# Kernel optimization log

Hardware: AMD Instinct MI355X
Metric: run time of the kernel (lower is better)

Reference implementation:

```python
import jax, jax.numpy as jnp
import numpy as np
from jax import lax

KH, KW = 3, 3
K = KH * KW
STRIDE, PAD, DIL = 1, 1, 1
CIN, COUT = 64, 64


def setup_inputs() -> dict:
    key = jax.random.key(0)
    k1, k2, k3, k4 = jax.random.split(key, 4)
    B, H, W = 8, 96, 96
    x = jax.random.normal(k1, (B, CIN, H, W), dtype=jnp.float32)
    # offset/mask conv params (small so sampled offsets stay near the grid)
    w_off = jax.random.normal(k2, (3 * K, CIN, KH, KW), dtype=jnp.float32) * 0.01
    b_off = jnp.zeros((3 * K,), dtype=jnp.float32)
    # main deformable conv weight, uniform(-stdv, stdv) like reset_parameters
    stdv = 1.0 / np.sqrt(CIN * KH * KW)
    weight = jax.random.uniform(k3, (COUT, CIN, KH, KW), dtype=jnp.float32,
                                minval=-stdv, maxval=stdv)
    bias = jax.random.normal(k4, (COUT,), dtype=jnp.float32) * 0.01
    return {"x": x, "w_off": w_off, "b_off": b_off, "weight": weight, "bias": bias}


def _bilinear_sample(img, ys, xs):
    # img: [C,H,W]; ys, xs: [K,Ho,Wo] float sample coords. Zero outside borders.
    C, H, W = img.shape
    y0 = jnp.floor(ys)
    x0 = jnp.floor(xs)
    wy1 = ys - y0  # weight for y0+1
    wx1 = xs - x0
    wy0 = 1.0 - wy1
    wx0 = 1.0 - wx1

    def gather(yi, xi):
        yc = jnp.clip(yi, 0, H - 1).astype(jnp.int32)
        xc = jnp.clip(xi, 0, W - 1).astype(jnp.int32)
        valid = ((yi >= 0) & (yi <= H - 1) & (xi >= 0) & (xi <= W - 1))
        # [C,K,Ho,Wo]
        return img[:, yc, xc] * valid.astype(img.dtype)[None]

    return (gather(y0, x0) * (wy0 * wx0)[None]
            + gather(y0, x0 + 1) * (wy0 * wx1)[None]
            + gather(y0 + 1, x0) * (wy1 * wx0)[None]
            + gather(y0 + 1, x0 + 1) * (wy1 * wx1)[None])


def reference(x, w_off, b_off, weight, bias):
    B, C, H, W = x.shape
    # offset/mask conv (same geometry as main conv)
    om = lax.conv_general_dilated(
        x, w_off, window_strides=(STRIDE, STRIDE),
        padding=[(PAD, PAD), (PAD, PAD)], rhs_dilation=(DIL, DIL),
        dimension_numbers=("NCHW", "OIHW", "NCHW")) + b_off[None, :, None, None]
    Ho, Wo = om.shape[2], om.shape[3]
    offset = om[:, :2 * K].reshape(B, K, 2, Ho, Wo)  # interleaved (dy,dx) per tap
    dy, dx = offset[:, :, 0], offset[:, :, 1]         # [B,K,Ho,Wo]
    mask = jax.nn.sigmoid(om[:, 2 * K:])              # [B,K,Ho,Wo]

    k = jnp.arange(K)
    ky = (k // KW).astype(jnp.float32) * DIL  # [K]
    kx = (k % KW).astype(jnp.float32) * DIL
    oy = jnp.arange(Ho, dtype=jnp.float32) * STRIDE - PAD  # [Ho]
    ox = jnp.arange(Wo, dtype=jnp.float32) * STRIDE - PAD  # [Wo]
    ys = oy[None, None, :, None] + ky[None, :, None, None] + dy  # [B,K,Ho,Wo]
    xs = ox[None, None, None, :] + kx[None, :, None, None] + dx

    sampled = jax.vmap(_bilinear_sample)(x, ys, xs)  # [B,C,K,Ho,Wo]
    w_r = weight.reshape(weight.shape[0], C, K)      # [O,C,K]
    out = jnp.einsum("bkhw,bckhw,ock->bohw", mask, sampled, w_r)
    return out + bias[None, :, None, None]
```

## Files before the change

kernel.cpp:

```cpp
#include <hip/hip_runtime.h>
#include <math.h>

typedef __bf16 b16x8 __attribute__((ext_vector_type(8)));
typedef float  f32x4 __attribute__((ext_vector_type(4)));

#define B_    8
#define CIN_  64
#define COUT_ 64
#define Hs    96
#define Ws    96
#define PLANE (Hs*Ws)
#define IMG   (CIN_*PLANE)
#define NP    (B_*PLANE)
#define NBLK  (NP/64)

#define WR 10
#define WC 24
#define WPIX (WR*WC)
#define WBYTES (WPIX*128)

__device__ __forceinline__ int swz(int bid) { return (bid & 7) * (NBLK / 8) + (bid >> 3); }

__global__ void prep_xpose(const float* __restrict__ x,
                           const float* __restrict__ weight, const float* __restrict__ w_off,
                           __bf16* __restrict__ xT,
                           __bf16* __restrict__ wAB, __bf16* __restrict__ wAO) {
    int bid = blockIdx.x;
    if (bid < 288) {
        int p = bid * 256 + threadIdx.x;
        int b = p / PLANE, r = p - b * PLANE;
        const float* src = x + b * IMG + r;
        __bf16 buf[64];
#pragma unroll
        for (int c = 0; c < 64; ++c) buf[c] = (__bf16)src[c * PLANE];
        b16x8* dst = (b16x8*)(xT + (size_t)p * 64);
#pragma unroll
        for (int j = 0; j < 8; ++j) dst[j] = ((const b16x8*)buf)[j];
    } else {
        int i = (bid - 288) * 256 + threadIdx.x;
        if (i < 36864) {
            int e = i & 7, lane = (i >> 3) & 63, mt = (i >> 9) & 3, ks = (i >> 11) & 1, k = i >> 12;
            int o = mt * 16 + (lane & 15);
            int c = ks * 32 + ((lane >> 4) << 3) + e;
            wAB[i] = (__bf16)weight[o * 576 + c * 9 + k];
        }
        if (i < 18432) {
            int e = i & 7, lane = (i >> 3) & 63, mt = (i >> 9) & 1, ks = (i >> 10) & 1, t = i >> 11;
            int ch = mt * 16 + (lane & 15);
            int c  = ks * 32 + ((lane >> 4) << 3) + e;
            wAO[i] = (ch < 27) ? (__bf16)w_off[ch * 576 + c * 9 + t] : (__bf16)(0.f);
        }
    }
}

__global__ __launch_bounds__(256, 4)
void deform_mfma(const __bf16* __restrict__ xT,
                 const __bf16* __restrict__ wAO,
                 const float* __restrict__ b_off,
                 const __bf16* __restrict__ wAB,
                 const float* __restrict__ bias,
                 float* __restrict__ out) {
    __shared__ __align__(16) unsigned char smemWin[WBYTES];
    __shared__ float omL[4][27 * 16];

    int tid  = threadIdx.x;
    int lane = tid & 63;
    int s    = __builtin_amdgcn_readfirstlane(tid >> 6);
    int n    = lane & 15;
    int q    = lane >> 4;

    int t    = swz(blockIdx.x);
    int b    = t / 144;
    int rem  = t - b * 144;
    int rq   = rem / 6;
    int ct   = rem - rq * 6;
    int h0   = rq * 4;
    int c0   = ct * 16;
    int hrow = h0 + s;
    int w    = c0 + n;

    const __bf16* xTimg = xT + (size_t)b * PLANE * 64;
    const __bf16* xTb   = xTimg + q * 8;

    const b16x8* wAOv = (const b16x8*)wAO;
    const b16x8* wABv = (const b16x8*)wAB;
    int boff = q * 16;

#define LDSRD(sl, off) (*(const b16x8*)(smemWin + (sl) * 128 + ((off) ^ (((sl) & 7) << 4))))

#pragma unroll
    for (int r2 = 0; r2 < 8; ++r2) {
        int idx = tid + r2 * 256;
        if (r2 < 7 || tid < (WPIX * 8 - 1792)) {
            int pix = idx >> 3, j = idx & 7;
            int yw = pix / WC, xw = pix - yw * WC;
            int ys = min(max(h0 - 3 + yw, 0), Hs - 1);
            int xs = min(max(c0 - 3 + xw, 0), Ws - 1);
            b16x8 v = *(const b16x8*)(xTimg + ((ys * Ws + xs) * 64) + j * 8);
            *(b16x8*)(smemWin + pix * 128 + ((j * 16) ^ ((pix & 7) << 4))) = v;
        }
    }
    __syncthreads();

    f32x4 accA0 = {0.f, 0.f, 0.f, 0.f};
    f32x4 accA1 = {0.f, 0.f, 0.f, 0.f};
    const b16x8 ZER = {};

#pragma unroll 3
    for (int tt = 0; tt < 9; ++tt) {
        int ky = tt / 3, kx = tt - ky * 3;
        int yy = hrow - 1 + ky, xx = w - 1 + kx;
        bool mk = (yy >= 0 && yy < Hs && xx >= 0 && xx < Ws);
        int sl = (s + 2 + ky) * WC + (n + 2 + kx);
        b16x8 bf0 = LDSRD(sl, boff);
        b16x8 bf1 = LDSRD(sl, boff + 64);
        bf0 = mk ? bf0 : ZER;
        bf1 = mk ? bf1 : ZER;
        b16x8 af0 = wAOv[((tt * 2 + 0) * 2 + 0) * 64 + lane];
        b16x8 af1 = wAOv[((tt * 2 + 0) * 2 + 1) * 64 + lane];
        b16x8 af2 = wAOv[((tt * 2 + 1) * 2 + 0) * 64 + lane];
        b16x8 af3 = wAOv[((tt * 2 + 1) * 2 + 1) * 64 + lane];
        accA0 = __builtin_amdgcn_mfma_f32_16x16x32_bf16(af0, bf0, accA0, 0, 0, 0);
        accA1 = __builtin_amdgcn_mfma_f32_16x16x32_bf16(af1, bf0, accA1, 0, 0, 0);
        accA0 = __builtin_amdgcn_mfma_f32_16x16x32_bf16(af2, bf1, accA0, 0, 0, 0);
        accA1 = __builtin_amdgcn_mfma_f32_16x16x32_bf16(af3, bf1, accA1, 0, 0, 0);
    }
    float* omW = &omL[s][0];
#pragma unroll
    for (int rg = 0; rg < 4; ++rg) { int ch = q * 4 + rg;      omW[ch * 16 + n] = accA0[rg] + b_off[ch]; }
#pragma unroll
    for (int rg = 0; rg < 4; ++rg) { int ch = 16 + q * 4 + rg; if (ch < 27) omW[ch * 16 + n] = accA1[rg] + b_off[ch]; }

    f32x4 acc0 = {0.f, 0.f, 0.f, 0.f};
    f32x4 acc1 = {0.f, 0.f, 0.f, 0.f};
    f32x4 acc2 = {0.f, 0.f, 0.f, 0.f};
    f32x4 acc3 = {0.f, 0.f, 0.f, 0.f};

#pragma unroll 3
    for (int k = 0; k < 9; ++k) {
        float dy = omW[(2 * k) * 16 + n];
        float dx = omW[(2 * k + 1) * 16 + n];
        float mo = omW[(18 + k) * 16 + n];

        float m  = 1.f / (1.f + __expf(-mo));
        int ky = k / 3, kx = k - ky * 3;
        float ysf = (float)(hrow - 1 + ky) + dy;
        float xsf = (float)(w    - 1 + kx) + dx;
        float y0f = floorf(ysf), x0f = floorf(xsf);
        float ly = ysf - y0f, lx = xsf - x0f;
        float hy = 1.f - ly, hx = 1.f - lx;
        int y0 = (int)y0f, x0 = (int)x0f, y1 = y0 + 1, x1 = x0 + 1;
        bool vy0 = (y0 >= 0) && (y0 < Hs), vy1 = (y1 >= 0) && (y1 < Hs);
        bool vx0 = (x0 >= 0) && (x0 < Ws), vx1 = (x1 >= 0) && (x1 < Ws);
        float W00 = (vy0 && vx0) ? m * hy * hx : 0.f;
        float W01 = (vy0 && vx1) ? m * hy * lx : 0.f;
        float W10 = (vy1 && vx0) ? m * ly * hx : 0.f;
        float W11 = (vy1 && vx1) ? m * ly * lx : 0.f;

        bool inw = (y0 >= h0 - 3) && (y1 <= h0 + 6) && (x0 >= c0 - 3) && (x1 <= c0 + 20);

        b16x8 e00, e01, e10, e11, o00, o01, o10, o11;
        if (inw) {
            int sl = (y0 - (h0 - 3)) * WC + (x0 - (c0 - 3));
            e00 = LDSRD(sl, boff);           o00 = LDSRD(sl, boff + 64);
            e01 = LDSRD(sl + 1, boff);       o01 = LDSRD(sl + 1, boff + 64);
            e10 = LDSRD(sl + WC, boff);      o10 = LDSRD(sl + WC, boff + 64);
            e11 = LDSRD(sl + WC + 1, boff);  o11 = LDSRD(sl + WC + 1, boff + 64);
        } else {
            int y0c = min(max(y0, 0), Hs - 1), y1c = min(max(y1, 0), Hs - 1);
            int x0c = min(max(x0, 0), Ws - 1), x1c = min(max(x1, 0), Ws - 1);
            const b16x8* P00 = (const b16x8*)(xTb + (y0c * Ws + x0c) * 64);
            const b16x8* P01 = (const b16x8*)(xTb + (y0c * Ws + x1c) * 64);
            const b16x8* P10 = (const b16x8*)(xTb + (y1c * Ws + x0c) * 64);
            const b16x8* P11 = (const b16x8*)(xTb + (y1c * Ws + x1c) * 64);
            e00 = P00[0]; o00 = P00[4];
            e01 = P01[0]; o01 = P01[4];
            e10 = P10[0]; o10 = P10[4];
            e11 = P11[0]; o11 = P11[4];
        }

        b16x8 a0 = wABv[(k * 8 + 0) * 64 + lane];
        b16x8 a1 = wABv[(k * 8 + 1) * 64 + lane];
        b16x8 a2 = wABv[(k * 8 + 2) * 64 + lane];
        b16x8 a3 = wABv[(k * 8 + 3) * 64 + lane];

        b16x8 fe;
#pragma unroll
        for (int j = 0; j < 8; ++j)
            fe[j] = (__bf16)((float)e00[j] * W00 + (float)e01[j] * W01 +
                             (float)e10[j] * W10 + (float)e11[j] * W11);
        acc0 = __builtin_amdgcn_mfma_f32_16x16x32_bf16(a0, fe, acc0, 0, 0, 0);
        acc1 = __builtin_amdgcn_mfma_f32_16x16x32_bf16(a1, fe, acc1, 0, 0, 0);
        acc2 = __builtin_amdgcn_mfma_f32_16x16x32_bf16(a2, fe, acc2, 0, 0, 0);
        acc3 = __builtin_amdgcn_mfma_f32_16x16x32_bf16(a3, fe, acc3, 0, 0, 0);

        b16x8 a4 = wABv[(k * 8 + 4) * 64 + lane];
        b16x8 a5 = wABv[(k * 8 + 5) * 64 + lane];
        b16x8 a6 = wABv[(k * 8 + 6) * 64 + lane];
        b16x8 a7 = wABv[(k * 8 + 7) * 64 + lane];

        b16x8 fo;
#pragma unroll
        for (int j = 0; j < 8; ++j)
            fo[j] = (__bf16)((float)o00[j] * W00 + (float)o01[j] * W01 +
                             (float)o10[j] * W10 + (float)o11[j] * W11);
        acc0 = __builtin_amdgcn_mfma_f32_16x16x32_bf16(a4, fo, acc0, 0, 0, 0);
        acc1 = __builtin_amdgcn_mfma_f32_16x16x32_bf16(a5, fo, acc1, 0, 0, 0);
        acc2 = __builtin_amdgcn_mfma_f32_16x16x32_bf16(a6, fo, acc2, 0, 0, 0);
        acc3 = __builtin_amdgcn_mfma_f32_16x16x32_bf16(a7, fo, acc3, 0, 0, 0);
    }
#undef LDSRD

    int ob = b * (COUT_ * PLANE) + hrow * Ws + w;
    f32x4 bs0 = *(const f32x4*)&bias[q * 4];
    f32x4 bs1 = *(const f32x4*)&bias[16 + q * 4];
    f32x4 bs2 = *(const f32x4*)&bias[32 + q * 4];
    f32x4 bs3 = *(const f32x4*)&bias[48 + q * 4];
#pragma unroll
    for (int rg = 0; rg < 4; ++rg) { int o =      q * 4 + rg; out[ob + o * PLANE] = acc0[rg] + bs0[rg]; }
#pragma unroll
    for (int rg = 0; rg < 4; ++rg) { int o = 16 + q * 4 + rg; out[ob + o * PLANE] = acc1[rg] + bs1[rg]; }
#pragma unroll
    for (int rg = 0; rg < 4; ++rg) { int o = 32 + q * 4 + rg; out[ob + o * PLANE] = acc2[rg] + bs2[rg]; }
#pragma unroll
    for (int rg = 0; rg < 4; ++rg) { int o = 48 + q * 4 + rg; out[ob + o * PLANE] = acc3[rg] + bs3[rg]; }
}

extern "C" void kernel_launch(void* const* d_in, const int* in_sizes, int n_in,
                              void* d_out, int out_size, void* d_ws, size_t ws_size,
                              hipStream_t stream) {
    const float* x      = (const float*)d_in[0];
    const float* w_off  = (const float*)d_in[1];
    const float* b_off  = (const float*)d_in[2];
    const float* weight = (const float*)d_in[3];
    const float* bias   = (const float*)d_in[4];
    float* out = (float*)d_out;

    char* ws = (char*)d_ws;
    __bf16* wAB = (__bf16*)ws;
    __bf16* wAO = (__bf16*)(ws + 73728);
    __bf16* xT  = (__bf16*)(ws + 131072);

    prep_xpose<<<432, 256, 0, stream>>>(x, weight, w_off, xT, wAB, wAO);
    deform_mfma<<<NBLK, 256, 0, stream>>>(xT, wAO, b_off, wAB, bias, out);
}
```

Before: 117.9 us.

## Shrink LDS halo window and software-pipeline bilinear tap loads across iterations

Shrinks the LDS input window from a 3-pixel to a 2-pixel halo (10x24 to 9x21 pixels, staged in exactly 6 passes with no tail guard), which cuts LDS footprint and staging loads. The deformable loop is restructured so the offset/weight math and even-half corner loads for tap k+1 are issued while tap k's odd half is being blended and fed to MFMA. The loop is no longer unrolled. Samples falling outside the smaller window take the global-memory fallback more often, and carrying the next tap's data raises register pressure.

```diff
diff --git a/kernel.cpp b/kernel.cpp
--- a/kernel.cpp
+++ b/kernel.cpp
@@ -14,10 +14,11 @@
 #define NP    (B_*PLANE)
 #define NBLK  (NP/64)
 
-#define WR 10
-#define WC 24
+#define WR 9
+#define WC 21
 #define WPIX (WR*WC)
-#define WBYTES (WPIX*128)
+#define WSTG 192
+#define WBYTES (WSTG*128)
 
 __device__ __forceinline__ int swz(int bid) { return (bid & 7) * (NBLK / 8) + (bid >> 3); }
 
@@ -86,19 +87,17 @@
     const b16x8* wABv = (const b16x8*)wAB;
     int boff = q * 16;
 
-#define LDSRD(sl, off) (*(const b16x8*)(smemWin + (sl) * 128 + ((off) ^ (((sl) & 7) << 4))))
-
-#pragma unroll
-    for (int r2 = 0; r2 < 8; ++r2) {
+#define LDSRD(sl_, off_) (*(const b16x8*)(smemWin + (sl_) * 128 + ((off_) ^ (((sl_) & 7) << 4))))
+
+#pragma unroll
+    for (int r2 = 0; r2 < 6; ++r2) {
         int idx = tid + r2 * 256;
-        if (r2 < 7 || tid < (WPIX * 8 - 1792)) {
-            int pix = idx >> 3, j = idx & 7;
-            int yw = pix / WC, xw = pix - yw * WC;
-            int ys = min(max(h0 - 3 + yw, 0), Hs - 1);
-            int xs = min(max(c0 - 3 + xw, 0), Ws - 1);
-            b16x8 v = *(const b16x8*)(xTimg + ((ys * Ws + xs) * 64) + j * 8);
-            *(b16x8*)(smemWin + pix * 128 + ((j * 16) ^ ((pix & 7) << 4))) = v;
-        }
+        int pix = idx >> 3, j = idx & 7;
+        int yw = pix / WC, xw = pix - yw * WC;
+        int ys = min(max(h0 - 2 + yw, 0), Hs - 1);
+        int xs = min(max(c0 - 2 + xw, 0), Ws - 1);
+        b16x8 v = *(const b16x8*)(xTimg + ((ys * Ws + xs) * 64) + j * 8);
+        *(b16x8*)(smemWin + pix * 128 + ((j * 16) ^ ((pix & 7) << 4))) = v;
     }
     __syncthreads();
 
@@ -111,9 +110,9 @@
         int ky = tt / 3, kx = tt - ky * 3;
         int yy = hrow - 1 + ky, xx = w - 1 + kx;
         bool mk = (yy >= 0 && yy < Hs && xx >= 0 && xx < Ws);
-        int sl = (s + 2 + ky) * WC + (n + 2 + kx);
-        b16x8 bf0 = LDSRD(sl, boff);
-        b16x8 bf1 = LDSRD(sl, boff + 64);
+        int slA = (s + 1 + ky) * WC + (n + 1 + kx);
+        b16x8 bf0 = LDSRD(slA, boff);
+        b16x8 bf1 = LDSRD(slA, boff + 64);
         bf0 = mk ? bf0 : ZER;
         bf1 = mk ? bf1 : ZER;
         b16x8 af0 = wAOv[((tt * 2 + 0) * 2 + 0) * 64 + lane];
@@ -136,53 +135,67 @@
     f32x4 acc2 = {0.f, 0.f, 0.f, 0.f};
     f32x4 acc3 = {0.f, 0.f, 0.f, 0.f};
 
-#pragma unroll 3
+    float W00, W01, W10, W11;
+    int   sl, y0r, x0r;
+    bool  inw;
+    b16x8 e00, e01, e10, e11;
+
+#define CALC_FROM(dy, dx, mo, kk) do {                                            \
+        float m  = 1.f / (1.f + __expf(-(mo)));                                   \
+        int ky = (kk) / 3, kx = (kk) - ky * 3;                                    \
+        float ysf = (float)(hrow - 1 + ky) + (dy);                                \
+        float xsf = (float)(w    - 1 + kx) + (dx);                                \
+        float y0f = floorf(ysf), x0f = floorf(xsf);                               \
+        float ly = ysf - y0f, lx = xsf - x0f;                                     \
+        float hy = 1.f - ly, hx = 1.f - lx;                                       \
+        y0r = (int)y0f; x0r = (int)x0f;                                           \
+        int y1 = y0r + 1, x1 = x0r + 1;                                           \
+        bool vy0 = (y0r >= 0) && (y0r < Hs), vy1 = (y1 >= 0) && (y1 < Hs);        \
+        bool vx0 = (x0r >= 0) && (x0r < Ws), vx1 = (x1 >= 0) && (x1 < Ws);        \
+        W00 = (vy0 && vx0) ? m * hy * hx : 0.f;                                   \
+        W01 = (vy0 && vx1) ? m * hy * lx : 0.f;                                   \
+        W10 = (vy1 && vx0) ? m * ly * hx : 0.f;                                   \
+        W11 = (vy1 && vx1) ? m * ly * lx : 0.f;                                   \
+        inw = (y0r >= h0 - 2) && (y1 <= h0 + 6) && (x0r >= c0 - 2) && (x1 <= c0 + 18); \
+        sl  = (y0r - (h0 - 2)) * WC + (x0r - (c0 - 2));                           \
+    } while (0)
+
+#define LOAD4(d0, d1, d2, d3, OFF, ELO) do {                                      \
+        if (inw) {                                                                \
+            d0 = LDSRD(sl, OFF);          d1 = LDSRD(sl + 1, OFF);                \
+            d2 = LDSRD(sl + WC, OFF);     d3 = LDSRD(sl + WC + 1, OFF);           \
+        } else {                                                                  \
+            int y0c = min(max(y0r, 0), Hs - 1), y1c = min(max(y0r + 1, 0), Hs - 1); \
+            int x0c = min(max(x0r, 0), Ws - 1), x1c = min(max(x0r + 1, 0), Ws - 1); \
+            d0 = *(const b16x8*)(xTb + (y0c * Ws + x0c) * 64 + (ELO));            \
+            d1 = *(const b16x8*)(xTb + (y0c * Ws + x1c) * 64 + (ELO));            \
+            d2 = *(const b16x8*)(xTb + (y1c * Ws + x0c) * 64 + (ELO));            \
+            d3 = *(const b16x8*)(xTb + (y1c * Ws + x1c) * 64 + (ELO));            \
+        }                                                                         \
+    } while (0)
+
+    {
+        float dy0 = omW[0 * 16 + n], dx0 = omW[1 * 16 + n], mo0 = omW[18 * 16 + n];
+        CALC_FROM(dy0, dx0, mo0, 0);
+        LOAD4(e00, e01, e10, e11, boff, 0);
+    }
+
+#pragma unroll 1
     for (int k = 0; k < 9; ++k) {
-        float dy = omW[(2 * k) * 16 + n];
-        float dx = omW[(2 * k + 1) * 16 + n];
-        float mo = omW[(18 + k) * 16 + n];
-
-        float m  = 1.f / (1.f + __expf(-mo));
-        int ky = k / 3, kx = k - ky * 3;
-        float ysf = (float)(hrow - 1 + ky) + dy;
-        float xsf = (float)(w    - 1 + kx) + dx;
-        float y0f = floorf(ysf), x0f = floorf(xsf);
-        float ly = ysf - y0f, lx = xsf - x0f;
-        float hy = 1.f - ly, hx = 1.f - lx;
-        int y0 = (int)y0f, x0 = (int)x0f, y1 = y0 + 1, x1 = x0 + 1;
-        bool vy0 = (y0 >= 0) && (y0 < Hs), vy1 = (y1 >= 0) && (y1 < Hs);
-        bool vx0 = (x0 >= 0) && (x0 < Ws), vx1 = (x1 >= 0) && (x1 < Ws);
-        float W00 = (vy0 && vx0) ? m * hy * hx : 0.f;
-        float W01 = (vy0 && vx1) ? m * hy * lx : 0.f;
-        float W10 = (vy1 && vx0) ? m * ly * hx : 0.f;
-        float W11 = (vy1 && vx1) ? m * ly * lx : 0.f;
-
-        bool inw = (y0 >= h0 - 3) && (y1 <= h0 + 6) && (x0 >= c0 - 3) && (x1 <= c0 + 20);
-
-        b16x8 e00, e01, e10, e11, o00, o01, o10, o11;
-        if (inw) {
-            int sl = (y0 - (h0 - 3)) * WC + (x0 - (c0 - 3));
-            e00 = LDSRD(sl, boff);           o00 = LDSRD(sl, boff + 64);
-            e01 = LDSRD(sl + 1, boff);       o01 = LDSRD(sl + 1, boff + 64);
-            e10 = LDSRD(sl + WC, boff);      o10 = LDSRD(sl + WC, boff + 64);
-            e11 = LDSRD(sl + WC + 1, boff);  o11 = LDSRD(sl + WC + 1, boff + 64);
-        } else {
-            int y0c = min(max(y0, 0), Hs - 1), y1c = min(max(y1, 0), Hs - 1);
-            int x0c = min(max(x0, 0), Ws - 1), x1c = min(max(x1, 0), Ws - 1);
-            const b16x8* P00 = (const b16x8*)(xTb + (y0c * Ws + x0c) * 64);
-            const b16x8* P01 = (const b16x8*)(xTb + (y0c * Ws + x1c) * 64);
-            const b16x8* P10 = (const b16x8*)(xTb + (y1c * Ws + x0c) * 64);
-            const b16x8* P11 = (const b16x8*)(xTb + (y1c * Ws + x1c) * 64);
-            e00 = P00[0]; o00 = P00[4];
-            e01 = P01[0]; o01 = P01[4];
-            e10 = P10[0]; o10 = P10[4];
-            e11 = P11[0]; o11 = P11[4];
-        }
-
         b16x8 a0 = wABv[(k * 8 + 0) * 64 + lane];
         b16x8 a1 = wABv[(k * 8 + 1) * 64 + lane];
         b16x8 a2 = wABv[(k * 8 + 2) * 64 + lane];
         b16x8 a3 = wABv[(k * 8 + 3) * 64 + lane];
+
+        b16x8 o00, o01, o10, o11;
+        LOAD4(o00, o01, o10, o11, boff + 64, 32);
+
+        int kn = (k < 8) ? (k + 1) : 8;
+        float dyN = omW[(2 * kn) * 16 + n];
+        float dxN = omW[(2 * kn + 1) * 16 + n];
+        float moN = omW[(18 + kn) * 16 + n];
+
+        float V00 = W00, V01 = W01, V10 = W10, V11 = W11;
 
         b16x8 fe;
 #pragma unroll
@@ -199,16 +212,23 @@
         b16x8 a6 = wABv[(k * 8 + 6) * 64 + lane];
         b16x8 a7 = wABv[(k * 8 + 7) * 64 + lane];
 
+        if (k < 8) {
+            CALC_FROM(dyN, dxN, moN, k + 1);
+            LOAD4(e00, e01, e10, e11, boff, 0);
+        }
+
         b16x8 fo;
 #pragma unroll
         for (int j = 0; j < 8; ++j)
-            fo[j] = (__bf16)((float)o00[j] * W00 + (float)o01[j] * W01 +
-                             (float)o10[j] * W10 + (float)o11[j] * W11);
+            fo[j] = (__bf16)((float)o00[j] * V00 + (float)o01[j] * V01 +
+                             (float)o10[j] * V10 + (float)o11[j] * V11);
         acc0 = __builtin_amdgcn_mfma_f32_16x16x32_bf16(a4, fo, acc0, 0, 0, 0);
         acc1 = __builtin_amdgcn_mfma_f32_16x16x32_bf16(a5, fo, acc1, 0, 0, 0);
         acc2 = __builtin_amdgcn_mfma_f32_16x16x32_bf16(a6, fo, acc2, 0, 0, 0);
         acc3 = __builtin_amdgcn_mfma_f32_16x16x32_bf16(a7, fo, acc3, 0, 0, 0);
     }
+#undef LOAD4
+#undef CALC_FROM
 #undef LDSRD
 
     int ob = b * (COUT_ * PLANE) + hrow * Ws + w;
```

Result: faster. 113.8 us (-3.5%).
